# Kernel optimization log

Measured on AMD Instinct MI355X. Metric: run time of the kernel, lower is better.

The kernel has to match this reference:

```python
import jax, jax.numpy as jnp
import numpy as np

N_NODES = 15
K = 5
L_IN = 1920
C_OUT = 256
L3 = L_IN - 3 * K + 3  # 1908
EPS = 1e-5


def setup_inputs() -> dict:
    key = jax.random.key(0)
    ks = jax.random.split(key, 18)
    B, E = 128, 56
    s = 0.05
    inp = {
        'X': jax.random.normal(ks[0], (B, N_NODES, L_IN), jnp.float32),
        'edge_index': jax.random.randint(ks[1], (2, E), 0, N_NODES),
        'edge_weight': jax.random.uniform(ks[2], (E,), jnp.float32),
        # grouped conv params (groups = N_NODES): per-group channels 1->16->32->1
        'conv1_w': jax.random.normal(ks[3], (16 * N_NODES, 1, K), jnp.float32) * s,
        'conv1_b': jnp.zeros((16 * N_NODES,), jnp.float32),
        'conv2_w': jax.random.normal(ks[4], (32 * N_NODES, 16, K), jnp.float32) * s,
        'conv2_b': jnp.zeros((32 * N_NODES,), jnp.float32),
        'conv3_w': jax.random.normal(ks[5], (N_NODES, 32, K), jnp.float32) * s,
        'conv3_b': jnp.zeros((N_NODES,), jnp.float32),
        # GCNConv: lin weight [out,in] + bias
        'gcn_w': jax.random.normal(ks[6], (C_OUT, L3), jnp.float32) * s,
        'gcn_b': jnp.zeros((C_OUT,), jnp.float32),
        'lin1_w': jax.random.normal(ks[7], (C_OUT, L_IN), jnp.float32) * s,
        'lin1_b': jnp.zeros((C_OUT,), jnp.float32),
        # GraphNorm params
        'gn_w': jnp.ones((C_OUT,), jnp.float32),
        'gn_b': jnp.zeros((C_OUT,), jnp.float32),
        'gn_ms': jnp.ones((C_OUT,), jnp.float32),
        'out_w': jax.random.normal(ks[8], (16, C_OUT), jnp.float32) * s,
        'out_b': jnp.zeros((16,), jnp.float32),
    }
    return inp


def _gconv(x, w, b):
    # grouped valid conv1d, NCH layout
    y = jax.lax.conv_general_dilated(
        x, w, window_strides=(1,), padding='VALID',
        dimension_numbers=('NCH', 'OIH', 'NCH'),
        feature_group_count=N_NODES)
    return y + b[None, :, None]


def _gcn(x, edge_index, edge_weight, W, b):
    # x: [B, N, L3]; batched GCNConv with shared edge structure (no per-t loop)
    src, dst = edge_index[0], edge_index[1]
    loop = jnp.arange(N_NODES)
    src = jnp.concatenate([src, loop])
    dst = jnp.concatenate([dst, loop])
    ew = jnp.concatenate([edge_weight, jnp.ones((N_NODES,), edge_weight.dtype)])
    deg = jnp.zeros((N_NODES,), ew.dtype).at[dst].add(ew)  # in-degree on target
    dinv = jnp.where(deg > 0, jax.lax.rsqrt(deg), 0.0)
    norm = dinv[src] * ew * dinv[dst]  # [E']
    xl = jnp.einsum('bnf,of->bno', x, W)  # [B, N, C_OUT]
    msg = norm[None, :, None] * xl[:, src, :]  # [B, E', C_OUT]
    out = jnp.zeros_like(xl).at[:, dst, :].add(msg)
    return out + b


def reference(X, edge_index, edge_weight, conv1_w, conv1_b, conv2_w, conv2_b,
              conv3_w, conv3_b, gcn_w, gcn_b, lin1_w, lin1_b, gn_w, gn_b,
              gn_ms, out_w, out_b):
    h = jax.nn.leaky_relu(_gconv(X, conv1_w, conv1_b), 0.01)
    h = jax.nn.leaky_relu(_gconv(h, conv2_w, conv2_b), 0.01)
    h = jax.nn.leaky_relu(_gconv(h, conv3_w, conv3_b), 0.01)  # [B, N, L3]
    T = _gcn(h, edge_index, edge_weight, gcn_w, gcn_b)  # [B, N, C_OUT]
    # GraphNorm with batch=None -> single graph over dim 0
    mean = T.mean(axis=0, keepdims=True)
    out = T - mean * gn_ms
    var = (out * out).mean(axis=0, keepdims=True)
    T = gn_w * out / jnp.sqrt(var + EPS) + gn_b
    T = jax.nn.elu(T + jnp.einsum('bnl,ol->bno', X, lin1_w) + lin1_b)
    output = T.mean(axis=1)  # global_mean_pool over nodes -> [B, C_OUT]
    class_output = output @ out_w.T + out_b  # [B, 16]
    return (output, class_output)
```

## Files before the change

kernel.cpp:

```cpp
#include <hip/hip_runtime.h>

typedef unsigned short u16;
typedef unsigned int   u32;

typedef short shortx8  __attribute__((ext_vector_type(8)));
typedef float floatx4  __attribute__((ext_vector_type(4)));
typedef u32   uintx4   __attribute__((ext_vector_type(4)));

typedef u32     u32a     __attribute__((may_alias));
typedef uintx4  uintx4a  __attribute__((may_alias));
typedef shortx8 shortx8a __attribute__((may_alias));

__device__ __forceinline__ u16 f2bf(float f){
  union { float f; u32 i; } v; v.f = f;
  return (u16)((v.i + 0x7fffu + ((v.i >> 16) & 1u)) >> 16);
}
__device__ __forceinline__ u16 f2bf_fast(float f){
  union { float f; u32 i; } v; v.f = f;
  return (u16)((v.i + 0x8000u) >> 16);
}
__device__ __forceinline__ u32 pack_bf16_fast(float lo, float hi){
  union { float f; u32 i; } a, b; a.f = lo; b.f = hi;
  return ((a.i + 0x8000u) >> 16) | ((b.i + 0x8000u) & 0xFFFF0000u);
}

__global__ void __launch_bounds__(256) prep(const float* __restrict__ lw,
                                            u16* __restrict__ lwb,
                                            const float* __restrict__ gw,
                                            u16* __restrict__ gwp){
  const int b = blockIdx.x, tid = threadIdx.x;
  if (b < 480){
    const int base = b*1024 + tid;
    #pragma unroll
    for (int u = 0; u < 4; ++u) lwb[base + 256*u] = f2bf(lw[base + 256*u]);
  } else {
    const int row = b - 480;
    for (int col = tid; col < 1920; col += 256)
      gwp[row*1920 + col] = (col < 1908) ? f2bf(gw[row*1908 + col]) : (u16)0;
  }
}

__global__ void __launch_bounds__(256) fused_conv(
    const float* __restrict__ X,
    const float* __restrict__ w1, const float* __restrict__ b1,
    const float* __restrict__ w2, const float* __restrict__ b2,
    const float* __restrict__ w3, const float* __restrict__ b3,
    u16* __restrict__ h3p, u16* __restrict__ Xb){
  const int tid  = threadIdx.x;
  const int node = blockIdx.z;
  const int p    = blockIdx.x * 60;
  const int b0   = blockIdx.y * 8;

  __shared__ __attribute__((aligned(16))) u16 sH1[4*1632];
  __shared__ __attribute__((aligned(16))) u16 sH2[4*2720];
  __shared__ __attribute__((aligned(16))) u16 sW2f[3072];
  __shared__ __attribute__((aligned(16))) u16 sW3f[160];
  __shared__ float sX[8*76];
  __shared__ float sW1[80], sB1[16], sB2[32];

  {
    const int bls = tid >> 5, i0 = tid & 31;
    const float* xrow = X  + (size_t)((b0 + bls)*15 + node)*1920;
    u16*        xbrow = Xb + (size_t)((b0 + bls)*15 + node)*1920;
    #pragma unroll
    for (int u = 0; u < 3; ++u){
      int i = i0 + 32*u;
      if (i < 76){
        int g = p + i;
        float xv = (i < 72 && g < 1920) ? xrow[g] : 0.f;
        sX[bls*76 + i] = xv;
        if (i < 60) xbrow[g] = f2bf_fast(xv);
      }
    }
    #pragma unroll
    for (int u = 0; u < 12; ++u){
      int d = tid + 256*u;
      int j = d & 7, mm = (d >> 3) & 15, qd = (d >> 7) & 3, t6 = d >> 9;
      int o = (t6 >= 3) ? 1 : 0, pi = t6 - 3*o;
      int tap = 2*pi + (qd >> 1), icc = (qd & 1)*8 + j, oc = o*16 + mm;
      sW2f[d] = (tap < 5) ? f2bf(w2[node*2560 + (oc*16 + icc)*5 + tap]) : (u16)0;
    }
    if (tid < 160){
      int icc = tid / 5, tp = tid - 5*icc;
      sW3f[tp*32 + icc] = f2bf(w3[node*160 + tid]);
    }
    if (tid < 80) sW1[tid] = w1[node*80 + tid];
    if (tid < 16) sB1[tid] = b1[node*16 + tid];
    if (tid < 32) sB2[tid] = b2[node*32 + tid];
  }
  __syncthreads();

  const int w = tid >> 6, lane = tid & 63;
  const int m = lane & 15, quad = lane >> 4;
  const int icb = (quad & 1)*8;
  const int tpo = quad >> 1;

  shortx8 a2[2][3];
  #pragma unroll
  for (int o = 0; o < 2; ++o)
    #pragma unroll
    for (int pi = 0; pi < 3; ++pi)
      a2[o][pi] = *(const shortx8a*)&sW2f[((o*3 + pi)*4 + quad)*128 + m*8];

  shortx8 a3[5];
  {
    const shortx8 zv = {0,0,0,0,0,0,0,0};
    #pragma unroll
    for (int tp = 0; tp < 5; ++tp){
      shortx8 t = *(const shortx8a*)&sW3f[tp*32 + quad*8];
      a3[tp] = (m == 0) ? t : zv;
    }
  }
  float biasr2[2][4];
  #pragma unroll
  for (int o = 0; o < 2; ++o)
    #pragma unroll
    for (int r = 0; r < 4; ++r)
      biasr2[o][r] = sB2[o*16 + quad*4 + r];
  const float b3v = b3[node];

  u16* h1w = sH1 + w*1632;
  u16* h2w = sH2 + w*2720;
  for (int i = lane; i < 160; i += 64) h2w[2560 + i] = 0;

  const int c1ic = (lane & 7)*2, c1t0 = (lane >> 3)*9;
  float wa[5], wb[5];
  #pragma unroll
  for (int k = 0; k < 5; ++k){ wa[k] = sW1[c1ic*5 + k]; wb[k] = sW1[c1ic*5 + 5 + k]; }
  const float ba = sB1[c1ic], bbv = sB1[c1ic + 1];

  for (int bb = 0; bb < 2; ++bb){
    const int bl = w + bb*4;

    {
      const float* xr = sX + bl*76;
      float x0 = xr[c1t0], x1 = xr[c1t0+1], x2 = xr[c1t0+2], x3 = xr[c1t0+3];
      #pragma unroll
      for (int i = 0; i < 9; ++i){
        const int t = c1t0 + i;
        float x4 = xr[t + 4];
        float va = ba  + wa[0]*x0 + wa[1]*x1 + wa[2]*x2 + wa[3]*x3 + wa[4]*x4;
        float vb = bbv + wb[0]*x0 + wb[1]*x1 + wb[2]*x2 + wb[3]*x3 + wb[4]*x4;
        va = va > 0.f ? va : 0.01f*va;
        vb = vb > 0.f ? vb : 0.01f*vb;
        if (t < 68) *(u32a*)(h1w + t*24 + c1ic) = pack_bf16_fast(va, vb);
        x0 = x1; x1 = x2; x2 = x3; x3 = x4;
      }
    }
    __syncthreads();

    #pragma unroll
    for (int q = 0; q < 4; ++q){
      const int trow = q*16 + m;
      shortx8 bf0 = *(const shortx8a*)(h1w + (trow     + tpo)*24 + icb);
      shortx8 bf1 = *(const shortx8a*)(h1w + (trow + 2 + tpo)*24 + icb);
      shortx8 bf2 = *(const shortx8a*)(h1w + (trow + 4      )*24 + icb);
      floatx4 ac0 = {0.f,0.f,0.f,0.f}, ac1 = {0.f,0.f,0.f,0.f};
      ac0 = __builtin_amdgcn_mfma_f32_16x16x32_bf16(a2[0][0], bf0, ac0, 0, 0, 0);
      ac1 = __builtin_amdgcn_mfma_f32_16x16x32_bf16(a2[1][0], bf0, ac1, 0, 0, 0);
      ac0 = __builtin_amdgcn_mfma_f32_16x16x32_bf16(a2[0][1], bf1, ac0, 0, 0, 0);
      ac1 = __builtin_amdgcn_mfma_f32_16x16x32_bf16(a2[1][1], bf1, ac1, 0, 0, 0);
      ac0 = __builtin_amdgcn_mfma_f32_16x16x32_bf16(a2[0][2], bf2, ac0, 0, 0, 0);
      ac1 = __builtin_amdgcn_mfma_f32_16x16x32_bf16(a2[1][2], bf2, ac1, 0, 0, 0);
      #pragma unroll
      for (int o = 0; o < 2; ++o){
        const floatx4& ac = o ? ac1 : ac0;
        float v0 = ac[0] + biasr2[o][0];
        float v1 = ac[1] + biasr2[o][1];
        float v2 = ac[2] + biasr2[o][2];
        float v3 = ac[3] + biasr2[o][3];
        v0 = v0 > 0.f ? v0 : 0.01f*v0;
        v1 = v1 > 0.f ? v1 : 0.01f*v1;
        v2 = v2 > 0.f ? v2 : 0.01f*v2;
        v3 = v3 > 0.f ? v3 : 0.01f*v3;
        u16* dst = h2w + trow*40 + o*16 + quad*4;
        *(u32a*)(dst)     = pack_bf16_fast(v0, v1);
        *(u32a*)(dst + 2) = pack_bf16_fast(v2, v3);
      }
    }
    __syncthreads();

    const int rg = (b0 + bl)*15 + node;
    #pragma unroll
    for (int nt = 0; nt < 4; ++nt){
      floatx4 acc3 = {0.f,0.f,0.f,0.f};
      if (lane < 16) acc3[0] = b3v;
      #pragma unroll
      for (int tp = 0; tp < 5; ++tp){
        shortx8 bfr = *(const shortx8a*)(h2w + (nt*16 + m + tp)*40 + quad*8);
        acc3 = __builtin_amdgcn_mfma_f32_16x16x32_bf16(a3[tp], bfr, acc3, 0, 0, 0);
      }
      const int tl = nt*16 + lane;
      if (lane < 16 && tl < 60){
        const int t3 = p + tl;
        float v = acc3[0];
        v = v > 0.f ? v : 0.01f*v;
        h3p[(size_t)rg*1920 + t3] = (t3 < 1908) ? f2bf_fast(v) : (u16)0;
      }
    }
  }
}

__global__ void __launch_bounds__(256) gemm_nt(
    const u16* __restrict__ A0, const u16* __restrict__ B0, float* __restrict__ O0,
    const u16* __restrict__ A1, const u16* __restrict__ B1, float* __restrict__ O1){
  const int job = blockIdx.z >> 1, kh = blockIdx.z & 1;
  const u16* A; const u16* Bm; float* O;
  if (job == 0){ A = A0; Bm = B0; O = O0; } else { A = A1; Bm = B1; O = O1; }
  __shared__ __attribute__((aligned(16))) u16 sA[64*40];
  __shared__ __attribute__((aligned(16))) u16 sB[64*40];
  const int tid = threadIdx.x;
  const int m0 = blockIdx.x*64, n0 = blockIdx.y*64;
  const int row = tid >> 2, kc = tid & 3;
  const int w = tid >> 6, lane = tid & 63;
  const int mo = (w & 1)*32, no = (w >> 1)*32;
  floatx4 acc[2][2];
  #pragma unroll
  for (int i = 0; i < 2; ++i)
    #pragma unroll
    for (int j = 0; j < 2; ++j)
      #pragma unroll
      for (int r = 0; r < 4; ++r) acc[i][j][r] = 0.f;

  const u16* ap = A  + (size_t)(m0 + row)*1920 + kh*960 + kc*8;
  const u16* bp = Bm + (size_t)(n0 + row)*1920 + kh*960 + kc*8;
  for (int kt = 0; kt < 30; ++kt){
    uintx4 va = *(const uintx4a*)ap;
    uintx4 vb = *(const uintx4a*)bp;
    ap += 32; bp += 32;
    *(uintx4a*)&sA[row*40 + kc*8] = va;
    *(uintx4a*)&sB[row*40 + kc*8] = vb;
    __syncthreads();
    const shortx8 af0 = *(const shortx8a*)&sA[(mo      + (lane & 15))*40 + (lane >> 4)*8];
    const shortx8 af1 = *(const shortx8a*)&sA[(mo + 16 + (lane & 15))*40 + (lane >> 4)*8];
    const shortx8 bf0 = *(const shortx8a*)&sB[(no      + (lane & 15))*40 + (lane >> 4)*8];
    const shortx8 bf1 = *(const shortx8a*)&sB[(no + 16 + (lane & 15))*40 + (lane >> 4)*8];
    acc[0][0] = __builtin_amdgcn_mfma_f32_16x16x32_bf16(af0, bf0, acc[0][0], 0, 0, 0);
    acc[0][1] = __builtin_amdgcn_mfma_f32_16x16x32_bf16(af0, bf1, acc[0][1], 0, 0, 0);
    acc[1][0] = __builtin_amdgcn_mfma_f32_16x16x32_bf16(af1, bf0, acc[1][0], 0, 0, 0);
    acc[1][1] = __builtin_amdgcn_mfma_f32_16x16x32_bf16(af1, bf1, acc[1][1], 0, 0, 0);
    __syncthreads();
  }
  #pragma unroll
  for (int mi = 0; mi < 2; ++mi)
    #pragma unroll
    for (int ni = 0; ni < 2; ++ni)
      #pragma unroll
      for (int r = 0; r < 4; ++r){
        int rr = m0 + mo + mi*16 + (lane >> 4)*4 + r;
        int cc = n0 + no + ni*16 + (lane & 15);
        atomicAdd(&O[(size_t)rr*256 + cc], acc[mi][ni][r]);
      }
}

__global__ void __launch_bounds__(256) gcn_agg(
    const float* __restrict__ xl, const int* __restrict__ ei,
    const float* __restrict__ ew, const float* __restrict__ gcn_b,
    float* __restrict__ Tpre){
  const int b = blockIdx.x, tid = threadIdx.x;
  __shared__ float sxl[15*256];
  __shared__ float s_deg[15], s_dinv[15], s_norm[71];
  __shared__ int   s_cnt[15], s_start[16], s_fill[15], s_srcl[71];
  if (tid < 15){ s_deg[tid] = 0.f; s_cnt[tid] = 0; s_fill[tid] = 0; }
  #pragma unroll
  for (int n = 0; n < 15; ++n)
    sxl[n*256 + tid] = xl[(size_t)(b*15 + n)*256 + tid];
  __syncthreads();
  int se = 0, de = 0; float we = 0.f;
  if (tid < 71){
    if (tid < 56){ se = ei[tid]; de = ei[56 + tid]; we = ew[tid]; }
    else         { se = tid - 56; de = tid - 56; we = 1.0f; }
    atomicAdd(&s_deg[de], we);
    atomicAdd(&s_cnt[de], 1);
  }
  __syncthreads();
  if (tid < 15) s_dinv[tid] = s_deg[tid] > 0.f ? rsqrtf(s_deg[tid]) : 0.f;
  if (tid == 0){
    int a = 0;
    for (int n = 0; n < 15; ++n){ s_start[n] = a; a += s_cnt[n]; }
    s_start[15] = a;
  }
  __syncthreads();
  if (tid < 71){
    float nrm = s_dinv[se]*we*s_dinv[de];
    int pos = s_start[de] + atomicAdd(&s_fill[de], 1);
    s_srcl[pos] = se; s_norm[pos] = nrm;
  }
  __syncthreads();
  const float gb = gcn_b[tid];
  for (int n = 0; n < 15; ++n){
    float acc = gb;
    const int e0 = s_start[n], e1 = s_start[n+1];
    for (int idx = e0; idx < e1; ++idx)
      acc += s_norm[idx]*sxl[s_srcl[idx]*256 + tid];
    Tpre[(size_t)(b*15 + n)*256 + tid] = acc;
  }
}

__global__ void __launch_bounds__(256) gn_stats(
    const float* __restrict__ Tpre, const float* __restrict__ gn_ms,
    const float* __restrict__ gn_w, float* __restrict__ moff, float* __restrict__ scal){
  const int n = blockIdx.x, c = threadIdx.x;
  float s = 0.f, s2 = 0.f;
  for (int b = 0; b < 128; ++b){
    float v = Tpre[(size_t)(b*15 + n)*256 + c];
    s += v; s2 += v*v;
  }
  const float mean = s*(1.f/128.f);
  const float mo = mean*gn_ms[c];
  float var = s2*(1.f/128.f) - 2.f*mo*mean + mo*mo;
  var = fmaxf(var, 0.f);
  moff[n*256 + c] = mo;
  scal[n*256 + c] = gn_w[c]*rsqrtf(var + 1e-5f);
}

__global__ void __launch_bounds__(256) finalize_k(
    const float* __restrict__ Tpre, const float* __restrict__ l1,
    const float* __restrict__ moff, const float* __restrict__ scal,
    const float* __restrict__ gn_b, const float* __restrict__ lin1_b,
    const float* __restrict__ out_w, const float* __restrict__ out_b,
    float* __restrict__ dout){
  const int b = blockIdx.x, tid = threadIdx.x;
  __shared__ float spool[256], spart[256];
  const float gnb = gn_b[tid], lb = lin1_b[tid];
  float acc = 0.f;
  #pragma unroll
  for (int n = 0; n < 15; ++n){
    float t = (Tpre[(size_t)(b*15 + n)*256 + tid] - moff[n*256 + tid])*scal[n*256 + tid]
              + gnb + l1[(size_t)(b*15 + n)*256 + tid] + lb;
    t = t > 0.f ? t : (__expf(t) - 1.f);
    acc += t;
  }
  const float pool = acc*(1.f/15.f);
  dout[b*256 + tid] = pool;
  spool[tid] = pool;
  __syncthreads();
  const int j = tid >> 4, q = tid & 15;
  float s = 0.f;
  for (int i = 0; i < 16; ++i){
    int cc = q + i*16;
    s += spool[cc]*out_w[j*256 + cc];
  }
  spart[tid] = s;
  __syncthreads();
  if (tid < 16){
    float tot = out_b[tid];
    #pragma unroll
    for (int i = 0; i < 16; ++i) tot += spart[tid*16 + i];
    dout[32768 + b*16 + tid] = tot;
  }
}

extern "C" void kernel_launch(void* const* d_in, const int* in_sizes, int n_in,
                              void* d_out, int out_size, void* d_ws, size_t ws_size,
                              hipStream_t stream){
  (void)in_sizes; (void)n_in; (void)out_size; (void)ws_size;
  const float* X    = (const float*)d_in[0];
  const int*   ei   = (const int*)d_in[1];
  const float* ew   = (const float*)d_in[2];
  const float* w1   = (const float*)d_in[3];
  const float* b1   = (const float*)d_in[4];
  const float* w2   = (const float*)d_in[5];
  const float* b2   = (const float*)d_in[6];
  const float* w3   = (const float*)d_in[7];
  const float* b3   = (const float*)d_in[8];
  const float* gw   = (const float*)d_in[9];
  const float* gb   = (const float*)d_in[10];
  const float* lw   = (const float*)d_in[11];
  const float* lb   = (const float*)d_in[12];
  const float* gnw  = (const float*)d_in[13];
  const float* gnb  = (const float*)d_in[14];
  const float* gnms = (const float*)d_in[15];
  const float* ow   = (const float*)d_in[16];
  const float* ob   = (const float*)d_in[17];

  char* ws = (char*)d_ws;
  u16*   h3p  = (u16*)(ws + 0);
  u16*   gwp  = (u16*)(ws + 7372800);
  u16*   Xb   = (u16*)(ws + 8355840);
  u16*   lwb  = (u16*)(ws + 15728640);
  float* xl   = (float*)(ws + 16711680);
  float* l1   = (float*)(ws + 18677760);
  float* Tpre = (float*)(ws + 0);
  float* moff = (float*)(ws + 7372800);
  float* scal = (float*)(ws + 7388160);

  hipMemsetAsync(ws + 16711680, 0, 3932160, stream);
  prep      <<<dim3(736),        dim3(256), 0, stream>>>(lw, lwb, gw, gwp);
  fused_conv<<<dim3(32, 16, 15), dim3(256), 0, stream>>>(X, w1, b1, w2, b2, w3, b3,
                                                         h3p, Xb);
  gemm_nt   <<<dim3(30, 4, 4),   dim3(256), 0, stream>>>(Xb, lwb, l1, h3p, gwp, xl);
  gcn_agg   <<<dim3(128),        dim3(256), 0, stream>>>(xl, ei, ew, gb, Tpre);
  gn_stats  <<<dim3(15),         dim3(256), 0, stream>>>(Tpre, gnms, gnw, moff, scal);
  finalize_k<<<dim3(128),        dim3(256), 0, stream>>>(Tpre, l1, moff, scal,
                                                         gnb, lb, ow, ob, (float*)d_out);
}
```

Before: 235.5 us.

## Widen conv blocks, double GEMM k-step, fold memset into prep, trim epilogue ops

Several unrelated changes are bundled. The conv kernel now runs 512-thread blocks covering 16 batch rows, amortising the per-block weight staging, and stores X in shared memory as bf16. The GEMM loads 64 k-elements per barrier instead of 32, halving the number of syncs. The hipMemset is folded into the prep kernel as a zeroing loop, and the leaky-relu and bf16 packing use fmax and perm intrinsics. Feeding bf16-rounded X into conv1 changes numerics slightly, and the larger shared-memory footprint per block may lower occupancy.

```diff
diff --git a/kernel.cpp b/kernel.cpp
--- a/kernel.cpp
+++ b/kernel.cpp
@@ -11,6 +11,9 @@
 typedef uintx4  uintx4a  __attribute__((may_alias));
 typedef shortx8 shortx8a __attribute__((may_alias));
 
+__device__ __forceinline__ float bf2f(u16 u){
+  union { u32 i; float f; } v; v.i = ((u32)u) << 16; return v.f;
+}
 __device__ __forceinline__ u16 f2bf(float f){
   union { float f; u32 i; } v; v.f = f;
   return (u16)((v.i + 0x7fffu + ((v.i >> 16) & 1u)) >> 16);
@@ -19,15 +22,17 @@
   union { float f; u32 i; } v; v.f = f;
   return (u16)((v.i + 0x8000u) >> 16);
 }
-__device__ __forceinline__ u32 pack_bf16_fast(float lo, float hi){
+__device__ __forceinline__ u32 pack2(float lo, float hi){
   union { float f; u32 i; } a, b; a.f = lo; b.f = hi;
-  return ((a.i + 0x8000u) >> 16) | ((b.i + 0x8000u) & 0xFFFF0000u);
-}
+  return __builtin_amdgcn_perm(b.i + 0x8000u, a.i + 0x8000u, 0x07060302u);
+}
+__device__ __forceinline__ float lrelu(float v){ return fmaxf(v, 0.01f*v); }
 
 __global__ void __launch_bounds__(256) prep(const float* __restrict__ lw,
                                             u16* __restrict__ lwb,
                                             const float* __restrict__ gw,
-                                            u16* __restrict__ gwp){
+                                            u16* __restrict__ gwp,
+                                            float* __restrict__ zbase){
   const int b = blockIdx.x, tid = threadIdx.x;
   if (b < 480){
     const int base = b*1024 + tid;
@@ -38,9 +43,15 @@
     for (int col = tid; col < 1920; col += 256)
       gwp[row*1920 + col] = (col < 1908) ? f2bf(gw[row*1908 + col]) : (u16)0;
   }
-}
-
-__global__ void __launch_bounds__(256) fused_conv(
+  const int gidx = b*256 + tid;
+  #pragma unroll
+  for (int u = 0; u < 6; ++u){
+    int i = gidx + u*188416;
+    if (i < 983040) zbase[i] = 0.f;
+  }
+}
+
+__global__ void __launch_bounds__(512, 4) fused_conv(
     const float* __restrict__ X,
     const float* __restrict__ w1, const float* __restrict__ b1,
     const float* __restrict__ w2, const float* __restrict__ b2,
@@ -49,13 +60,13 @@
   const int tid  = threadIdx.x;
   const int node = blockIdx.z;
   const int p    = blockIdx.x * 60;
-  const int b0   = blockIdx.y * 8;
-
-  __shared__ __attribute__((aligned(16))) u16 sH1[4*1632];
-  __shared__ __attribute__((aligned(16))) u16 sH2[4*2720];
+  const int b0   = blockIdx.y * 16;
+
+  __shared__ __attribute__((aligned(16))) u16 sH1[8*1632];
+  __shared__ __attribute__((aligned(16))) u16 sH2[8*2720];
   __shared__ __attribute__((aligned(16))) u16 sW2f[3072];
   __shared__ __attribute__((aligned(16))) u16 sW3f[160];
-  __shared__ float sX[8*76];
+  __shared__ u16 sXb[16*76];
   __shared__ float sW1[80], sB1[16], sB2[32];
 
   {
@@ -68,13 +79,14 @@
       if (i < 76){
         int g = p + i;
         float xv = (i < 72 && g < 1920) ? xrow[g] : 0.f;
-        sX[bls*76 + i] = xv;
-        if (i < 60) xbrow[g] = f2bf_fast(xv);
-      }
-    }
-    #pragma unroll
-    for (int u = 0; u < 12; ++u){
-      int d = tid + 256*u;
+        u16 xb = f2bf_fast(xv);
+        sXb[bls*76 + i] = xb;
+        if (i < 60) xbrow[g] = xb;
+      }
+    }
+    #pragma unroll
+    for (int u = 0; u < 6; ++u){
+      int d = tid + 512*u;
       int j = d & 7, mm = (d >> 3) & 15, qd = (d >> 7) & 3, t6 = d >> 9;
       int o = (t6 >= 3) ? 1 : 0, pi = t6 - 3*o;
       int tap = 2*pi + (qd >> 1), icc = (qd & 1)*8 + j, oc = o*16 + mm;
@@ -130,20 +142,20 @@
   const float ba = sB1[c1ic], bbv = sB1[c1ic + 1];
 
   for (int bb = 0; bb < 2; ++bb){
-    const int bl = w + bb*4;
+    const int bl = w + bb*8;
 
     {
-      const float* xr = sX + bl*76;
-      float x0 = xr[c1t0], x1 = xr[c1t0+1], x2 = xr[c1t0+2], x3 = xr[c1t0+3];
+      const u16* xr = sXb + bl*76;
+      float x0 = bf2f(xr[c1t0]),   x1 = bf2f(xr[c1t0+1]);
+      float x2 = bf2f(xr[c1t0+2]), x3 = bf2f(xr[c1t0+3]);
       #pragma unroll
       for (int i = 0; i < 9; ++i){
         const int t = c1t0 + i;
-        float x4 = xr[t + 4];
+        float x4 = bf2f(xr[t + 4]);
         float va = ba  + wa[0]*x0 + wa[1]*x1 + wa[2]*x2 + wa[3]*x3 + wa[4]*x4;
         float vb = bbv + wb[0]*x0 + wb[1]*x1 + wb[2]*x2 + wb[3]*x3 + wb[4]*x4;
-        va = va > 0.f ? va : 0.01f*va;
-        vb = vb > 0.f ? vb : 0.01f*vb;
-        if (t < 68) *(u32a*)(h1w + t*24 + c1ic) = pack_bf16_fast(va, vb);
+        va = lrelu(va); vb = lrelu(vb);
+        if (t < 68) *(u32a*)(h1w + t*24 + c1ic) = pack2(va, vb);
         x0 = x1; x1 = x2; x2 = x3; x3 = x4;
       }
     }
@@ -165,17 +177,13 @@
       #pragma unroll
       for (int o = 0; o < 2; ++o){
         const floatx4& ac = o ? ac1 : ac0;
-        float v0 = ac[0] + biasr2[o][0];
-        float v1 = ac[1] + biasr2[o][1];
-        float v2 = ac[2] + biasr2[o][2];
-        float v3 = ac[3] + biasr2[o][3];
-        v0 = v0 > 0.f ? v0 : 0.01f*v0;
-        v1 = v1 > 0.f ? v1 : 0.01f*v1;
-        v2 = v2 > 0.f ? v2 : 0.01f*v2;
-        v3 = v3 > 0.f ? v3 : 0.01f*v3;
+        float v0 = lrelu(ac[0] + biasr2[o][0]);
+        float v1 = lrelu(ac[1] + biasr2[o][1]);
+        float v2 = lrelu(ac[2] + biasr2[o][2]);
+        float v3 = lrelu(ac[3] + biasr2[o][3]);
         u16* dst = h2w + trow*40 + o*16 + quad*4;
-        *(u32a*)(dst)     = pack_bf16_fast(v0, v1);
-        *(u32a*)(dst + 2) = pack_bf16_fast(v2, v3);
+        *(u32a*)(dst)     = pack2(v0, v1);
+        *(u32a*)(dst + 2) = pack2(v2, v3);
       }
     }
     __syncthreads();
@@ -193,8 +201,7 @@
       const int tl = nt*16 + lane;
       if (lane < 16 && tl < 60){
         const int t3 = p + tl;
-        float v = acc3[0];
-        v = v > 0.f ? v : 0.01f*v;
+        float v = lrelu(acc3[0]);
         h3p[(size_t)rg*1920 + t3] = (t3 < 1908) ? f2bf_fast(v) : (u16)0;
       }
     }
@@ -207,12 +214,13 @@
   const int job = blockIdx.z >> 1, kh = blockIdx.z & 1;
   const u16* A; const u16* Bm; float* O;
   if (job == 0){ A = A0; Bm = B0; O = O0; } else { A = A1; Bm = B1; O = O1; }
-  __shared__ __attribute__((aligned(16))) u16 sA[64*40];
-  __shared__ __attribute__((aligned(16))) u16 sB[64*40];
+  __shared__ __attribute__((aligned(16))) u16 sA[64*88];
+  __shared__ __attribute__((aligned(16))) u16 sB[64*88];
   const int tid = threadIdx.x;
   const int m0 = blockIdx.x*64, n0 = blockIdx.y*64;
   const int row = tid >> 2, kc = tid & 3;
   const int w = tid >> 6, lane = tid & 63;
+  const int m = lane & 15, quad = lane >> 4;
   const int mo = (w & 1)*32, no = (w >> 1)*32;
   floatx4 acc[2][2];
   #pragma unroll
@@ -224,21 +232,28 @@
 
   const u16* ap = A  + (size_t)(m0 + row)*1920 + kh*960 + kc*8;
   const u16* bp = Bm + (size_t)(n0 + row)*1920 + kh*960 + kc*8;
-  for (int kt = 0; kt < 30; ++kt){
-    uintx4 va = *(const uintx4a*)ap;
-    uintx4 vb = *(const uintx4a*)bp;
-    ap += 32; bp += 32;
-    *(uintx4a*)&sA[row*40 + kc*8] = va;
-    *(uintx4a*)&sB[row*40 + kc*8] = vb;
+  for (int kt = 0; kt < 15; ++kt){
+    uintx4 va0 = *(const uintx4a*)ap;
+    uintx4 va1 = *(const uintx4a*)(ap + 32);
+    uintx4 vb0 = *(const uintx4a*)bp;
+    uintx4 vb1 = *(const uintx4a*)(bp + 32);
+    ap += 64; bp += 64;
+    *(uintx4a*)&sA[row*88 + kc*8]      = va0;
+    *(uintx4a*)&sA[row*88 + 32 + kc*8] = va1;
+    *(uintx4a*)&sB[row*88 + kc*8]      = vb0;
+    *(uintx4a*)&sB[row*88 + 32 + kc*8] = vb1;
     __syncthreads();
-    const shortx8 af0 = *(const shortx8a*)&sA[(mo      + (lane & 15))*40 + (lane >> 4)*8];
-    const shortx8 af1 = *(const shortx8a*)&sA[(mo + 16 + (lane & 15))*40 + (lane >> 4)*8];
-    const shortx8 bf0 = *(const shortx8a*)&sB[(no      + (lane & 15))*40 + (lane >> 4)*8];
-    const shortx8 bf1 = *(const shortx8a*)&sB[(no + 16 + (lane & 15))*40 + (lane >> 4)*8];
-    acc[0][0] = __builtin_amdgcn_mfma_f32_16x16x32_bf16(af0, bf0, acc[0][0], 0, 0, 0);
-    acc[0][1] = __builtin_amdgcn_mfma_f32_16x16x32_bf16(af0, bf1, acc[0][1], 0, 0, 0);
-    acc[1][0] = __builtin_amdgcn_mfma_f32_16x16x32_bf16(af1, bf0, acc[1][0], 0, 0, 0);
-    acc[1][1] = __builtin_amdgcn_mfma_f32_16x16x32_bf16(af1, bf1, acc[1][1], 0, 0, 0);
+    #pragma unroll
+    for (int ks = 0; ks < 64; ks += 32){
+      const shortx8 af0 = *(const shortx8a*)&sA[(mo      + m)*88 + ks + quad*8];
+      const shortx8 af1 = *(const shortx8a*)&sA[(mo + 16 + m)*88 + ks + quad*8];
+      const shortx8 bf0 = *(const shortx8a*)&sB[(no      + m)*88 + ks + quad*8];
+      const shortx8 bf1 = *(const shortx8a*)&sB[(no + 16 + m)*88 + ks + quad*8];
+      acc[0][0] = __builtin_amdgcn_mfma_f32_16x16x32_bf16(af0, bf0, acc[0][0], 0, 0, 0);
+      acc[0][1] = __builtin_amdgcn_mfma_f32_16x16x32_bf16(af0, bf1, acc[0][1], 0, 0, 0);
+      acc[1][0] = __builtin_amdgcn_mfma_f32_16x16x32_bf16(af1, bf0, acc[1][0], 0, 0, 0);
+      acc[1][1] = __builtin_amdgcn_mfma_f32_16x16x32_bf16(af1, bf1, acc[1][1], 0, 0, 0);
+    }
     __syncthreads();
   }
   #pragma unroll
@@ -247,8 +262,8 @@
     for (int ni = 0; ni < 2; ++ni)
       #pragma unroll
       for (int r = 0; r < 4; ++r){
-        int rr = m0 + mo + mi*16 + (lane >> 4)*4 + r;
-        int cc = n0 + no + ni*16 + (lane & 15);
+        int rr = m0 + mo + mi*16 + quad*4 + r;
+        int cc = n0 + no + ni*16 + m;
         atomicAdd(&O[(size_t)rr*256 + cc], acc[mi][ni][r]);
       }
 }
@@ -385,9 +400,9 @@
   float* moff = (float*)(ws + 7372800);
   float* scal = (float*)(ws + 7388160);
 
-  hipMemsetAsync(ws + 16711680, 0, 3932160, stream);
-  prep      <<<dim3(736),        dim3(256), 0, stream>>>(lw, lwb, gw, gwp);
-  fused_conv<<<dim3(32, 16, 15), dim3(256), 0, stream>>>(X, w1, b1, w2, b2, w3, b3,
+  prep      <<<dim3(736),        dim3(256), 0, stream>>>(lw, lwb, gw, gwp,
+                                                         (float*)(ws + 16711680));
+  fused_conv<<<dim3(32, 8, 15),  dim3(512), 0, stream>>>(X, w1, b1, w2, b2, w3, b3,
                                                          h3p, Xb);
   gemm_nt   <<<dim3(30, 4, 4),   dim3(256), 0, stream>>>(Xb, lwb, l1, h3p, gwp, xl);
   gcn_agg   <<<dim3(128),        dim3(256), 0, stream>>>(xl, ei, ew, gb, Tpre);
```

Result: faster. 219.4 us (-6.9%).
